# Optimization experiments

Measured on AMD Instinct MI355X. Metric: run time of the kernel, lower is better.

The kernel has to match this reference:

```python
import jax, jax.numpy as jnp
import numpy as np

NEG_SLOPE = 0.1
K = 3  # kernel_size

def lrelu(x):
    return jnp.where(x >= 0, x, NEG_SLOPE * x)

def setup_inputs() -> dict:
    key = jax.random.key(0)
    ks = jax.random.split(key, 10)
    B, C, H, W = 16, 64, 128, 128
    DEG, RED = 512, 8
    s = 0.02
    return {
        "feat": jax.random.normal(ks[0], (B, C, H, W), jnp.float32),
        "deg": jax.random.normal(ks[1], (B, DEG, 8, 8), jnp.float32),
        # adaptive_size: Linear(deg_fsize -> C), no bias; torch weight [out,in]
        "W_size": jax.random.normal(ks[2], (C, DEG), jnp.float32) * s,
        # kernel net: Linear(C -> C//red), Linear(C//red -> C*K*K)
        "W_k1": jax.random.normal(ks[3], (C // RED, C), jnp.float32) * s,
        "W_k2": jax.random.normal(ks[4], (C * K * K, C // RED), jnp.float32) * s,
        # 1x1 conv C_in -> C_out with bias (stored as [out,in])
        "W_conv": jax.random.normal(ks[5], (C, C), jnp.float32) * s,
        "b_conv": jax.random.normal(ks[6], (C,), jnp.float32) * s,
        # CA layer: 1x1 conv deg_fsize -> C, then C -> C//red -> C
        "W_ac": jax.random.normal(ks[7], (C, DEG), jnp.float32) * s,
        "W_du1": jax.random.normal(ks[8], (C // RED, C), jnp.float32) * s,
        "W_du2": jax.random.normal(ks[9], (C, C // RED), jnp.float32) * s,
    }

def reference(feat, deg, W_size, W_k1, W_k2, W_conv, b_conv, W_ac, W_du1, W_du2):
    b, c, h, w = feat.shape
    # degradation pooled to a vector: AdaptiveAvgPool2d((1,1)) == mean over HW
    dvec = deg.mean(axis=(2, 3))                      # [B, deg_fsize]
    f = dvec @ W_size.T                               # [B, C]
    # per-sample dynamic depthwise kernels
    kern = lrelu(f @ W_k1.T) @ W_k2.T                 # [B, C*K*K]
    kern = kern.reshape(b * c, 1, K, K)               # [B*C, 1, K, K]
    out = jax.lax.conv_general_dilated(
        feat.reshape(1, b * c, h, w), kern,
        window_strides=(1, 1), padding=[((K - 1) // 2,) * 2] * 2,
        feature_group_count=b * c,
        dimension_numbers=("NCHW", "OIHW", "NCHW"))
    out = lrelu(out).reshape(b, c, h, w)
    # trailing 1x1 conv with bias
    out = jnp.einsum("bchw,oc->bohw", out, W_conv) + b_conv[None, :, None, None]
    # CA branch
    fa = dvec @ W_ac.T                                # [B, C]
    att = jax.nn.sigmoid(lrelu(fa @ W_du1.T) @ W_du2.T)  # [B, C_out]
    return out + feat * att[:, :, None, None]
```

## Files before the change

### kernel.cpp

```cpp
#include <hip/hip_runtime.h>
#include <math.h>

#define NEG_SLOPE 0.1f

typedef __attribute__((ext_vector_type(8))) short short8;
typedef __attribute__((ext_vector_type(4))) float floatx4;

__device__ __forceinline__ float lrelu(float x) { return x >= 0.0f ? x : NEG_SLOPE * x; }

__device__ __forceinline__ unsigned short f2bf(float x) {
  unsigned u = __float_as_uint(x);
  return (unsigned short)((u + 0x7fffu + ((u >> 16) & 1u)) >> 16);
}

__device__ __forceinline__ float wave_sum64(float v) {
  #pragma unroll
  for (int s = 32; s > 0; s >>= 1) v += __shfl_xor(v, s, 64);
  return v;
}

__global__ __launch_bounds__(256) void prep_kernel(
    const float* __restrict__ deg, const float* __restrict__ W_size,
    const float* __restrict__ W_k1, const float* __restrict__ W_k2,
    const float* __restrict__ W_ac, const float* __restrict__ W_du1,
    const float* __restrict__ W_du2, float* __restrict__ kern_ws,
    float* __restrict__ att_ws) {
  const int b = blockIdx.x;
  const int t = threadIdx.x;
  __shared__ float dvec[512];
  __shared__ float fbuf[64], fabuf[64];
  __shared__ float t1s[8], t2s[8];

  const float* degb = deg + (size_t)b * 32768;
  const int q = t & 3, r0 = t >> 2;

  float rs[8];
  #pragma unroll
  for (int u = 0; u < 8; ++u) {
    const float* rp = degb + (size_t)(r0 + u * 64) * 64 + q * 16;
    float4 x0 = *(const float4*)(rp);
    float4 x1 = *(const float4*)(rp + 4);
    float4 x2 = *(const float4*)(rp + 8);
    float4 x3 = *(const float4*)(rp + 12);
    rs[u] = (x0.x + x0.y + x0.z + x0.w) + (x1.x + x1.y + x1.z + x1.w) +
            (x2.x + x2.y + x2.z + x2.w) + (x3.x + x3.y + x3.z + x3.w);
  }
  #pragma unroll
  for (int u = 0; u < 8; ++u) {
    float s = rs[u];
    s += __shfl_xor(s, 1, 64);
    s += __shfl_xor(s, 2, 64);
    if (q == 0) dvec[r0 + u * 64] = s * (1.0f / 64.0f);
  }
  __syncthreads();

  {
    const int c = t >> 2;
    const float* ws = W_size + (size_t)c * 512;
    const float* wa = W_ac + (size_t)c * 512;
    float p1 = 0.0f, p2 = 0.0f;
    #pragma unroll 4
    for (int k = 0; k < 32; ++k) {
      const int e = q * 4 + k * 16;
      float4 d  = *(const float4*)&dvec[e];
      float4 w1 = *(const float4*)(ws + e);
      float4 w2 = *(const float4*)(wa + e);
      p1 += d.x * w1.x + d.y * w1.y + d.z * w1.z + d.w * w1.w;
      p2 += d.x * w2.x + d.y * w2.y + d.z * w2.z + d.w * w2.w;
    }
    p1 += __shfl_xor(p1, 1, 64); p1 += __shfl_xor(p1, 2, 64);
    p2 += __shfl_xor(p2, 1, 64); p2 += __shfl_xor(p2, 2, 64);
    if (q == 0) { fbuf[c] = p1; fabuf[c] = p2; }
  }
  __syncthreads();

  const int wave = t >> 6, lane = t & 63;
  if (wave == 0) {
    float v = fbuf[lane];
    #pragma unroll
    for (int rr = 0; rr < 8; ++rr) {
      float p = wave_sum64(v * W_k1[rr * 64 + lane]);
      if (lane == 0) t1s[rr] = lrelu(p);
    }
  } else if (wave == 1) {
    float v = fabuf[lane];
    #pragma unroll
    for (int rr = 0; rr < 8; ++rr) {
      float p = wave_sum64(v * W_du1[rr * 64 + lane]);
      if (lane == 0) t2s[rr] = lrelu(p);
    }
  }
  __syncthreads();

  for (int i = t; i < 576; i += 256) {
    float4 wa0 = *(const float4*)&W_k2[i * 8];
    float4 wa1 = *(const float4*)&W_k2[i * 8 + 4];
    float s = t1s[0] * wa0.x + t1s[1] * wa0.y + t1s[2] * wa0.z + t1s[3] * wa0.w +
              t1s[4] * wa1.x + t1s[5] * wa1.y + t1s[6] * wa1.z + t1s[7] * wa1.w;
    kern_ws[b * 576 + i] = s;
  }
  if (t < 64) {
    float4 wa0 = *(const float4*)&W_du2[t * 8];
    float4 wa1 = *(const float4*)&W_du2[t * 8 + 4];
    float s = t2s[0] * wa0.x + t2s[1] * wa0.y + t2s[2] * wa0.z + t2s[3] * wa0.w +
              t2s[4] * wa1.x + t2s[5] * wa1.y + t2s[6] * wa1.z + t2s[7] * wa1.w;
    att_ws[b * 64 + t] = 1.0f / (1.0f + expf(-s));
  }
}

__global__ __launch_bounds__(256, 4) void fused_kernel(
    const float* __restrict__ feat, const float* __restrict__ W_conv,
    const float* __restrict__ b_conv, const float* __restrict__ kern_ws,
    const float* __restrict__ att_ws, float* __restrict__ out) {
  const int L = blockIdx.y * 128 + blockIdx.x;
  const int xcd = L & 7;
  const int rr_ = L >> 3;
  const int h = xcd * 16 + (rr_ & 15);
  const int b = rr_ >> 4;

  const int t = threadIdx.x;

  __shared__ __align__(16) unsigned short zT[128 * 72];
  __shared__ __align__(16) unsigned short wt[64 * 72];
  __shared__ float ks[576];
  __shared__ float atts[64];
  __shared__ float bcs[64];

  {
    const int o = t >> 2;
    const int c0 = (t & 3) * 16;
    const float* wp = W_conv + o * 64 + c0;
    float4 a0 = *(const float4*)(wp);
    float4 a1 = *(const float4*)(wp + 4);
    float4 a2 = *(const float4*)(wp + 8);
    float4 a3 = *(const float4*)(wp + 12);
    const int sw = (o >> 2) & 7;
    short8 p0, p1;
    p0[0] = f2bf(a0.x); p0[1] = f2bf(a0.y); p0[2] = f2bf(a0.z); p0[3] = f2bf(a0.w);
    p0[4] = f2bf(a1.x); p0[5] = f2bf(a1.y); p0[6] = f2bf(a1.z); p0[7] = f2bf(a1.w);
    p1[0] = f2bf(a2.x); p1[1] = f2bf(a2.y); p1[2] = f2bf(a2.z); p1[3] = f2bf(a2.w);
    p1[4] = f2bf(a3.x); p1[5] = f2bf(a3.y); p1[6] = f2bf(a3.z); p1[7] = f2bf(a3.w);
    const int kc0 = (c0 >> 3) ^ sw;
    const int kc1 = ((c0 >> 3) + 1) ^ sw;
    *(short8*)&wt[o * 72 + kc0 * 8] = p0;
    *(short8*)&wt[o * 72 + kc1 * 8] = p1;
  }
  for (int i = t; i < 576; i += 256) ks[i] = kern_ws[b * 576 + i];
  if (t < 64) { atts[t] = att_ws[b * 64 + t]; bcs[t] = b_conv[t]; }
  __syncthreads();

  const size_t base_b = (size_t)b * 64 * 128 * 128;

  {
    const int c8 = t & 7;
    const int gg = t >> 3;
    const int w0 = gg * 4;
    const int swz = gg & 7;

    #pragma unroll
    for (int it = 0; it < 8; ++it) {
      const int c = c8 + 8 * it;
      const float* kc = &ks[c * 9];
      const float k0 = kc[0], k1 = kc[1], k2 = kc[2];
      const float k3 = kc[3], k4 = kc[4], k5 = kc[5];
      const float k6 = kc[6], k7 = kc[7], k8 = kc[8];
      float a0 = 0.0f, a1 = 0.0f, a2 = 0.0f, a3 = 0.0f;
      const float* fc = feat + base_b + (size_t)c * 16384;

      auto row_acc = [&](const float* rowp, float ka, float kb, float kcv) {
        float4 m = *(const float4*)(rowp + w0);
        float left  = (w0 > 0)   ? rowp[w0 - 1] : 0.0f;
        float right = (w0 < 124) ? rowp[w0 + 4] : 0.0f;
        a0 += ka * left + kb * m.x + kcv * m.y;
        a1 += ka * m.x  + kb * m.y + kcv * m.z;
        a2 += ka * m.y  + kb * m.z + kcv * m.w;
        a3 += ka * m.z  + kb * m.w + kcv * right;
      };
      if (h > 0)   row_acc(fc + (size_t)(h - 1) * 128, k0, k1, k2);
                   row_acc(fc + (size_t)h * 128,       k3, k4, k5);
      if (h < 127) row_acc(fc + (size_t)(h + 1) * 128, k6, k7, k8);

      const int cbase = ((it ^ swz) * 8) + c8;
      zT[(w0 + 0) * 72 + cbase] = f2bf(lrelu(a0));
      zT[(w0 + 1) * 72 + cbase] = f2bf(lrelu(a1));
      zT[(w0 + 2) * 72 + cbase] = f2bf(lrelu(a2));
      zT[(w0 + 3) * 72 + cbase] = f2bf(lrelu(a3));
    }
  }
  __syncthreads();

  {
    const int lane = t & 63, wave = t >> 6;
    const int r = lane & 15, q = lane >> 4;
    const int m0 = wave * 16;

    short8 afrag[2];
    #pragma unroll
    for (int ksp = 0; ksp < 2; ++ksp) {
      const int o = m0 + r;
      const int kc = (ksp * 4 + q) ^ ((o >> 2) & 7);
      afrag[ksp] = *(const short8*)&wt[o * 72 + kc * 8];
    }

    floatx4 acc[8];
    #pragma unroll
    for (int nt = 0; nt < 8; ++nt) acc[nt] = (floatx4){0.f, 0.f, 0.f, 0.f};

    #pragma unroll
    for (int nt = 0; nt < 8; ++nt) {
      const int w = nt * 16 + r;
      const int sw = (w >> 2) & 7;
      #pragma unroll
      for (int ksp = 0; ksp < 2; ++ksp) {
        const int kc = (ksp * 4 + q) ^ sw;
        short8 bfrag = *(const short8*)&zT[w * 72 + kc * 8];
        acc[nt] = __builtin_amdgcn_mfma_f32_16x16x32_bf16(afrag[ksp], bfrag,
                                                          acc[nt], 0, 0, 0);
      }
    }

    #pragma unroll
    for (int nt = 0; nt < 8; ++nt) {
      const int w = nt * 16 + r;
      #pragma unroll
      for (int reg = 0; reg < 4; ++reg) {
        const int o = m0 + q * 4 + reg;
        const size_t idx = base_b + (size_t)o * 16384 + (size_t)h * 128 + w;
        out[idx] = acc[nt][reg] + bcs[o] + atts[o] * feat[idx];
      }
    }
  }
}

extern "C" void kernel_launch(void* const* d_in, const int* in_sizes, int n_in,
                              void* d_out, int out_size, void* d_ws, size_t ws_size,
                              hipStream_t stream) {
  const float* feat   = (const float*)d_in[0];
  const float* deg    = (const float*)d_in[1];
  const float* W_size = (const float*)d_in[2];
  const float* W_k1   = (const float*)d_in[3];
  const float* W_k2   = (const float*)d_in[4];
  const float* W_conv = (const float*)d_in[5];
  const float* b_conv = (const float*)d_in[6];
  const float* W_ac   = (const float*)d_in[7];
  const float* W_du1  = (const float*)d_in[8];
  const float* W_du2  = (const float*)d_in[9];
  float* out = (float*)d_out;

  float* kern_ws = (float*)d_ws;
  float* att_ws  = kern_ws + 16 * 576;

  prep_kernel<<<16, 256, 0, stream>>>(deg, W_size, W_k1, W_k2, W_ac, W_du1,
                                      W_du2, kern_ws, att_ws);
  fused_kernel<<<dim3(128, 16), 256, 0, stream>>>(feat, W_conv, b_conv,
                                                  kern_ws, att_ws, out);
}
```

Before: 183.6 us.

## Split prep into three parallel kernels and restructure fused conv with two rows per block

```diff
diff --git a/kernel.cpp b/kernel.cpp
--- a/kernel.cpp
+++ b/kernel.cpp
@@ -4,6 +4,7 @@
 #define NEG_SLOPE 0.1f
 
 typedef __attribute__((ext_vector_type(8))) short short8;
+typedef __attribute__((ext_vector_type(4))) short short4v;
 typedef __attribute__((ext_vector_type(4))) float floatx4;
 
 __device__ __forceinline__ float lrelu(float x) { return x >= 0.0f ? x : NEG_SLOPE * x; }
@@ -19,71 +20,78 @@
   return v;
 }
 
-__global__ __launch_bounds__(256) void prep_kernel(
-    const float* __restrict__ deg, const float* __restrict__ W_size,
+__global__ __launch_bounds__(256) void prep1_kernel(
+    const float* __restrict__ deg, float* __restrict__ dvec_ws) {
+  const int k = blockIdx.x;
+  const int b = k >> 2, quar = k & 3;
+  const int t = threadIdx.x;
+  const int rw = t >> 1, half = t & 1;
+  const int d = quar * 128 + rw;
+  const float* p = deg + (size_t)b * 32768 + (size_t)d * 64 + half * 32;
+  float4 x0 = *(const float4*)(p);
+  float4 x1 = *(const float4*)(p + 4);
+  float4 x2 = *(const float4*)(p + 8);
+  float4 x3 = *(const float4*)(p + 12);
+  float4 x4 = *(const float4*)(p + 16);
+  float4 x5 = *(const float4*)(p + 20);
+  float4 x6 = *(const float4*)(p + 24);
+  float4 x7 = *(const float4*)(p + 28);
+  float s = (x0.x + x0.y + x0.z + x0.w) + (x1.x + x1.y + x1.z + x1.w) +
+            (x2.x + x2.y + x2.z + x2.w) + (x3.x + x3.y + x3.z + x3.w) +
+            (x4.x + x4.y + x4.z + x4.w) + (x5.x + x5.y + x5.z + x5.w) +
+            (x6.x + x6.y + x6.z + x6.w) + (x7.x + x7.y + x7.z + x7.w);
+  s += __shfl_xor(s, 1, 64);
+  if (half == 0) dvec_ws[b * 512 + d] = s * (1.0f / 64.0f);
+}
+
+__global__ __launch_bounds__(256) void prep2_kernel(
+    const float* __restrict__ dvec_ws, const float* __restrict__ W_size,
+    const float* __restrict__ W_ac, float* __restrict__ f_ws,
+    float* __restrict__ fa_ws) {
+  const int k = blockIdx.x;
+  const int b = k >> 2, cq = k & 3;
+  const int t = threadIdx.x;
+  const int cl = t >> 4, sub = t & 15;
+  const int c = cq * 16 + cl;
+  const float* dv = dvec_ws + b * 512;
+  const float* w1 = W_size + (size_t)c * 512;
+  const float* w2 = W_ac + (size_t)c * 512;
+  float p1 = 0.0f, p2 = 0.0f;
+  #pragma unroll
+  for (int kk = 0; kk < 8; ++kk) {
+    const int e = sub * 4 + kk * 64;
+    float4 d  = *(const float4*)(dv + e);
+    float4 a  = *(const float4*)(w1 + e);
+    float4 bq = *(const float4*)(w2 + e);
+    p1 += d.x * a.x + d.y * a.y + d.z * a.z + d.w * a.w;
+    p2 += d.x * bq.x + d.y * bq.y + d.z * bq.z + d.w * bq.w;
+  }
+  #pragma unroll
+  for (int s = 1; s < 16; s <<= 1) {
+    p1 += __shfl_xor(p1, s, 64);
+    p2 += __shfl_xor(p2, s, 64);
+  }
+  if (sub == 0) { f_ws[b * 64 + c] = p1; fa_ws[b * 64 + c] = p2; }
+}
+
+__global__ __launch_bounds__(256) void prep3_kernel(
+    const float* __restrict__ f_ws, const float* __restrict__ fa_ws,
     const float* __restrict__ W_k1, const float* __restrict__ W_k2,
-    const float* __restrict__ W_ac, const float* __restrict__ W_du1,
-    const float* __restrict__ W_du2, float* __restrict__ kern_ws,
-    float* __restrict__ att_ws) {
+    const float* __restrict__ W_du1, const float* __restrict__ W_du2,
+    float* __restrict__ kern_ws, float* __restrict__ att_ws) {
   const int b = blockIdx.x;
   const int t = threadIdx.x;
-  __shared__ float dvec[512];
-  __shared__ float fbuf[64], fabuf[64];
   __shared__ float t1s[8], t2s[8];
-
-  const float* degb = deg + (size_t)b * 32768;
-  const int q = t & 3, r0 = t >> 2;
-
-  float rs[8];
-  #pragma unroll
-  for (int u = 0; u < 8; ++u) {
-    const float* rp = degb + (size_t)(r0 + u * 64) * 64 + q * 16;
-    float4 x0 = *(const float4*)(rp);
-    float4 x1 = *(const float4*)(rp + 4);
-    float4 x2 = *(const float4*)(rp + 8);
-    float4 x3 = *(const float4*)(rp + 12);
-    rs[u] = (x0.x + x0.y + x0.z + x0.w) + (x1.x + x1.y + x1.z + x1.w) +
-            (x2.x + x2.y + x2.z + x2.w) + (x3.x + x3.y + x3.z + x3.w);
-  }
-  #pragma unroll
-  for (int u = 0; u < 8; ++u) {
-    float s = rs[u];
-    s += __shfl_xor(s, 1, 64);
-    s += __shfl_xor(s, 2, 64);
-    if (q == 0) dvec[r0 + u * 64] = s * (1.0f / 64.0f);
-  }
-  __syncthreads();
-
-  {
-    const int c = t >> 2;
-    const float* ws = W_size + (size_t)c * 512;
-    const float* wa = W_ac + (size_t)c * 512;
-    float p1 = 0.0f, p2 = 0.0f;
-    #pragma unroll 4
-    for (int k = 0; k < 32; ++k) {
-      const int e = q * 4 + k * 16;
-      float4 d  = *(const float4*)&dvec[e];
-      float4 w1 = *(const float4*)(ws + e);
-      float4 w2 = *(const float4*)(wa + e);
-      p1 += d.x * w1.x + d.y * w1.y + d.z * w1.z + d.w * w1.w;
-      p2 += d.x * w2.x + d.y * w2.y + d.z * w2.z + d.w * w2.w;
-    }
-    p1 += __shfl_xor(p1, 1, 64); p1 += __shfl_xor(p1, 2, 64);
-    p2 += __shfl_xor(p2, 1, 64); p2 += __shfl_xor(p2, 2, 64);
-    if (q == 0) { fbuf[c] = p1; fabuf[c] = p2; }
-  }
-  __syncthreads();
-
   const int wave = t >> 6, lane = t & 63;
   if (wave == 0) {
-    float v = fbuf[lane];
+    float v = f_ws[b * 64 + lane];
     #pragma unroll
     for (int rr = 0; rr < 8; ++rr) {
       float p = wave_sum64(v * W_k1[rr * 64 + lane]);
       if (lane == 0) t1s[rr] = lrelu(p);
     }
   } else if (wave == 1) {
-    float v = fabuf[lane];
+    float v = fa_ws[b * 64 + lane];
     #pragma unroll
     for (int rr = 0; rr < 8; ++rr) {
       float p = wave_sum64(v * W_du1[rr * 64 + lane]);
@@ -91,13 +99,12 @@
     }
   }
   __syncthreads();
-
   for (int i = t; i < 576; i += 256) {
     float4 wa0 = *(const float4*)&W_k2[i * 8];
     float4 wa1 = *(const float4*)&W_k2[i * 8 + 4];
-    float s = t1s[0] * wa0.x + t1s[1] * wa0.y + t1s[2] * wa0.z + t1s[3] * wa0.w +
-              t1s[4] * wa1.x + t1s[5] * wa1.y + t1s[6] * wa1.z + t1s[7] * wa1.w;
-    kern_ws[b * 576 + i] = s;
+    kern_ws[b * 576 + i] =
+        t1s[0] * wa0.x + t1s[1] * wa0.y + t1s[2] * wa0.z + t1s[3] * wa0.w +
+        t1s[4] * wa1.x + t1s[5] * wa1.y + t1s[6] * wa1.z + t1s[7] * wa1.w;
   }
   if (t < 64) {
     float4 wa0 = *(const float4*)&W_du2[t * 8];
@@ -112,11 +119,12 @@
     const float* __restrict__ feat, const float* __restrict__ W_conv,
     const float* __restrict__ b_conv, const float* __restrict__ kern_ws,
     const float* __restrict__ att_ws, float* __restrict__ out) {
-  const int L = blockIdx.y * 128 + blockIdx.x;
-  const int xcd = L & 7;
-  const int rr_ = L >> 3;
-  const int h = xcd * 16 + (rr_ & 15);
-  const int b = rr_ >> 4;
+  const int bid = blockIdx.x;
+  const int xcd = bid & 7;
+  const int idx = bid >> 3;
+  const int b = idx >> 3;
+  const int sub = idx & 7;
+  const int h_base = xcd * 16 + sub * 2;
 
   const int t = threadIdx.x;
 
@@ -134,13 +142,13 @@
     float4 a1 = *(const float4*)(wp + 4);
     float4 a2 = *(const float4*)(wp + 8);
     float4 a3 = *(const float4*)(wp + 12);
-    const int sw = (o >> 2) & 7;
+    const int sw = ((o >> 2) ^ (o >> 5)) & 7;
     short8 p0, p1;
     p0[0] = f2bf(a0.x); p0[1] = f2bf(a0.y); p0[2] = f2bf(a0.z); p0[3] = f2bf(a0.w);
     p0[4] = f2bf(a1.x); p0[5] = f2bf(a1.y); p0[6] = f2bf(a1.z); p0[7] = f2bf(a1.w);
     p1[0] = f2bf(a2.x); p1[1] = f2bf(a2.y); p1[2] = f2bf(a2.z); p1[3] = f2bf(a2.w);
     p1[4] = f2bf(a3.x); p1[5] = f2bf(a3.y); p1[6] = f2bf(a3.z); p1[7] = f2bf(a3.w);
-    const int kc0 = (c0 >> 3) ^ sw;
+    const int kc0 = ((c0 >> 3) + 0) ^ sw;
     const int kc1 = ((c0 >> 3) + 1) ^ sw;
     *(short8*)&wt[o * 72 + kc0 * 8] = p0;
     *(short8*)&wt[o * 72 + kc1 * 8] = p1;
@@ -150,85 +158,143 @@
   __syncthreads();
 
   const size_t base_b = (size_t)b * 64 * 128 * 128;
-
-  {
-    const int c8 = t & 7;
-    const int gg = t >> 3;
-    const int w0 = gg * 4;
-    const int swz = gg & 7;
+  const int lane = t & 63, wave = t >> 6;
+  const int cq = t >> 5;
+  const int gg = t & 31;
+  const int w0 = gg * 4;
+  const int swz = (gg ^ (gg >> 3)) & 7;
+  const float4 zf4 = {0.f, 0.f, 0.f, 0.f};
+
+  #pragma unroll 1
+  for (int ti = 0; ti < 2; ++ti) {
+    const int h = h_base + ti;
+    const bool hgt0 = (h > 0), hlt = (h < 127);
+    const float* fbase = feat + base_b + (size_t)h * 128 + w0;
 
     #pragma unroll
-    for (int it = 0; it < 8; ++it) {
-      const int c = c8 + 8 * it;
-      const float* kc = &ks[c * 9];
-      const float k0 = kc[0], k1 = kc[1], k2 = kc[2];
-      const float k3 = kc[3], k4 = kc[4], k5 = kc[5];
-      const float k6 = kc[6], k7 = kc[7], k8 = kc[8];
-      float a0 = 0.0f, a1 = 0.0f, a2 = 0.0f, a3 = 0.0f;
-      const float* fc = feat + base_b + (size_t)c * 16384;
-
-      auto row_acc = [&](const float* rowp, float ka, float kb, float kcv) {
-        float4 m = *(const float4*)(rowp + w0);
-        float left  = (w0 > 0)   ? rowp[w0 - 1] : 0.0f;
-        float right = (w0 < 124) ? rowp[w0 + 4] : 0.0f;
-        a0 += ka * left + kb * m.x + kcv * m.y;
-        a1 += ka * m.x  + kb * m.y + kcv * m.z;
-        a2 += ka * m.y  + kb * m.z + kcv * m.w;
-        a3 += ka * m.z  + kb * m.w + kcv * right;
-      };
-      if (h > 0)   row_acc(fc + (size_t)(h - 1) * 128, k0, k1, k2);
-                   row_acc(fc + (size_t)h * 128,       k3, k4, k5);
-      if (h < 127) row_acc(fc + (size_t)(h + 1) * 128, k6, k7, k8);
-
-      const int cbase = ((it ^ swz) * 8) + c8;
-      zT[(w0 + 0) * 72 + cbase] = f2bf(lrelu(a0));
-      zT[(w0 + 1) * 72 + cbase] = f2bf(lrelu(a1));
-      zT[(w0 + 2) * 72 + cbase] = f2bf(lrelu(a2));
-      zT[(w0 + 3) * 72 + cbase] = f2bf(lrelu(a3));
+    for (int it = 0; it < 2; ++it) {
+      const int c0 = cq * 4 + it * 32;
+      float4 top[4], mid[4], bot[4];
+      #pragma unroll
+      for (int j = 0; j < 4; ++j) {
+        const float* p = fbase + (size_t)(c0 + j) * 16384;
+        mid[j] = *(const float4*)p;
+        top[j] = hgt0 ? *(const float4*)(p - 128) : zf4;
+        bot[j] = hlt  ? *(const float4*)(p + 128) : zf4;
+      }
+      unsigned short sres[4][4];
+      #pragma unroll
+      for (int j = 0; j < 4; ++j) {
+        const float* kv = &ks[(c0 + j) * 9];
+        const float k0 = kv[0], k1 = kv[1], k2 = kv[2];
+        const float k3 = kv[3], k4 = kv[4], k5 = kv[5];
+        const float k6 = kv[6], k7 = kv[7], k8 = kv[8];
+        float a0 = 0.f, a1 = 0.f, a2 = 0.f, a3 = 0.f;
+        {
+          float4 m = top[j];
+          float lf = __shfl(m.w, lane - 1, 64); if (gg == 0)  lf = 0.f;
+          float rt = __shfl(m.x, lane + 1, 64); if (gg == 31) rt = 0.f;
+          a0 += k0 * lf  + k1 * m.x + k2 * m.y;
+          a1 += k0 * m.x + k1 * m.y + k2 * m.z;
+          a2 += k0 * m.y + k1 * m.z + k2 * m.w;
+          a3 += k0 * m.z + k1 * m.w + k2 * rt;
+        }
+        {
+          float4 m = mid[j];
+          float lf = __shfl(m.w, lane - 1, 64); if (gg == 0)  lf = 0.f;
+          float rt = __shfl(m.x, lane + 1, 64); if (gg == 31) rt = 0.f;
+          a0 += k3 * lf  + k4 * m.x + k5 * m.y;
+          a1 += k3 * m.x + k4 * m.y + k5 * m.z;
+          a2 += k3 * m.y + k4 * m.z + k5 * m.w;
+          a3 += k3 * m.z + k4 * m.w + k5 * rt;
+        }
+        {
+          float4 m = bot[j];
+          float lf = __shfl(m.w, lane - 1, 64); if (gg == 0)  lf = 0.f;
+          float rt = __shfl(m.x, lane + 1, 64); if (gg == 31) rt = 0.f;
+          a0 += k6 * lf  + k7 * m.x + k8 * m.y;
+          a1 += k6 * m.x + k7 * m.y + k8 * m.z;
+          a2 += k6 * m.y + k7 * m.z + k8 * m.w;
+          a3 += k6 * m.z + k7 * m.w + k8 * rt;
+        }
+        sres[j][0] = f2bf(lrelu(a0));
+        sres[j][1] = f2bf(lrelu(a1));
+        sres[j][2] = f2bf(lrelu(a2));
+        sres[j][3] = f2bf(lrelu(a3));
+      }
+      const int chunk = (cq >> 1) + it * 4;
+      const int kcs = ((chunk ^ swz) * 8) + (cq & 1) * 4;
+      #pragma unroll
+      for (int i = 0; i < 4; ++i) {
+        short4v sv;
+        sv[0] = (short)sres[0][i]; sv[1] = (short)sres[1][i];
+        sv[2] = (short)sres[2][i]; sv[3] = (short)sres[3][i];
+        *(short4v*)&zT[(w0 + i) * 72 + kcs] = sv;
+      }
     }
-  }
-  __syncthreads();
-
-  {
-    const int lane = t & 63, wave = t >> 6;
-    const int r = lane & 15, q = lane >> 4;
-    const int m0 = wave * 16;
-
-    short8 afrag[2];
-    #pragma unroll
-    for (int ksp = 0; ksp < 2; ++ksp) {
-      const int o = m0 + r;
-      const int kc = (ksp * 4 + q) ^ ((o >> 2) & 7);
-      afrag[ksp] = *(const short8*)&wt[o * 72 + kc * 8];
+    __syncthreads();
+
+    {
+      const int r = lane & 15, q = lane >> 4;
+
+      short8 az[2][2];
+      #pragma unroll
+      for (int wm2 = 0; wm2 < 2; ++wm2) {
+        const int w = (wave * 2 + wm2) * 16 + r;
+        const int sz = ((w >> 2) ^ (w >> 5)) & 7;
+        #pragma unroll
+        for (int ksp = 0; ksp < 2; ++ksp) {
+          const int kc = (ksp * 4 + q) ^ sz;
+          az[wm2][ksp] = *(const short8*)&zT[w * 72 + kc * 8];
+        }
+      }
+      short8 bw[4][2];
+      #pragma unroll
+      for (int nt = 0; nt < 4; ++nt) {
+        const int o = nt * 16 + r;
+        const int so = ((o >> 2) ^ (o >> 5)) & 7;
+        #pragma unroll
+        for (int ksp = 0; ksp < 2; ++ksp) {
+          const int kc = (ksp * 4 + q) ^ so;
+          bw[nt][ksp] = *(const short8*)&wt[o * 72 + kc * 8];
+        }
+      }
+
+      floatx4 acc[2][4];
+      #pragma unroll
+      for (int wm2 = 0; wm2 < 2; ++wm2)
+        #pragma unroll
+        for (int nt = 0; nt < 4; ++nt) acc[wm2][nt] = (floatx4){0.f, 0.f, 0.f, 0.f};
+
+      #pragma unroll
+      for (int wm2 = 0; wm2 < 2; ++wm2)
+        #pragma unroll
+        for (int nt = 0; nt < 4; ++nt)
+          #pragma unroll
+          for (int ksp = 0; ksp < 2; ++ksp)
+            acc[wm2][nt] = __builtin_amdgcn_mfma_f32_16x16x32_bf16(
+                az[wm2][ksp], bw[nt][ksp], acc[wm2][nt], 0, 0, 0);
+
+      #pragma unroll
+      for (int wm2 = 0; wm2 < 2; ++wm2) {
+        const int wb = (wave * 2 + wm2) * 16 + q * 4;
+        #pragma unroll
+        for (int nt = 0; nt < 4; ++nt) {
+          const int o = nt * 16 + r;
+          const size_t off = base_b + (size_t)o * 16384 + (size_t)h * 128 + wb;
+          float4 fv = *(const float4*)(feat + off);
+          const float at = atts[o], bo = bcs[o];
+          floatx4 a = acc[wm2][nt];
+          float4 ov;
+          ov.x = a[0] + bo + at * fv.x;
+          ov.y = a[1] + bo + at * fv.y;
+          ov.z = a[2] + bo + at * fv.z;
+          ov.w = a[3] + bo + at * fv.w;
+          *(float4*)(out + off) = ov;
+        }
+      }
     }
-
-    floatx4 acc[8];
-    #pragma unroll
-    for (int nt = 0; nt < 8; ++nt) acc[nt] = (floatx4){0.f, 0.f, 0.f, 0.f};
-
-    #pragma unroll
-    for (int nt = 0; nt < 8; ++nt) {
-      const int w = nt * 16 + r;
-      const int sw = (w >> 2) & 7;
-      #pragma unroll
-      for (int ksp = 0; ksp < 2; ++ksp) {
-        const int kc = (ksp * 4 + q) ^ sw;
-        short8 bfrag = *(const short8*)&zT[w * 72 + kc * 8];
-        acc[nt] = __builtin_amdgcn_mfma_f32_16x16x32_bf16(afrag[ksp], bfrag,
-                                                          acc[nt], 0, 0, 0);
-      }
-    }
-
-    #pragma unroll
-    for (int nt = 0; nt < 8; ++nt) {
-      const int w = nt * 16 + r;
-      #pragma unroll
-      for (int reg = 0; reg < 4; ++reg) {
-        const int o = m0 + q * 4 + reg;
-        const size_t idx = base_b + (size_t)o * 16384 + (size_t)h * 128 + w;
-        out[idx] = acc[nt][reg] + bcs[o] + atts[o] * feat[idx];
-      }
-    }
+    if (ti == 0) __syncthreads();
   }
 }
 
@@ -247,11 +313,16 @@
   const float* W_du2  = (const float*)d_in[9];
   float* out = (float*)d_out;
 
-  float* kern_ws = (float*)d_ws;
+  float* dvec_ws = (float*)d_ws;
+  float* f_ws    = dvec_ws + 16 * 512;
+  float* fa_ws   = f_ws + 16 * 64;
+  float* kern_ws = fa_ws + 16 * 64;
   float* att_ws  = kern_ws + 16 * 576;
 
-  prep_kernel<<<16, 256, 0, stream>>>(deg, W_size, W_k1, W_k2, W_ac, W_du1,
-                                      W_du2, kern_ws, att_ws);
-  fused_kernel<<<dim3(128, 16), 256, 0, stream>>>(feat, W_conv, b_conv,
-                                                  kern_ws, att_ws, out);
-}
+  prep1_kernel<<<64, 256, 0, stream>>>(deg, dvec_ws);
+  prep2_kernel<<<64, 256, 0, stream>>>(dvec_ws, W_size, W_ac, f_ws, fa_ws);
+  prep3_kernel<<<16, 256, 0, stream>>>(f_ws, fa_ws, W_k1, W_k2, W_du1, W_du2,
+                                       kern_ws, att_ws);
+  fused_kernel<<<1024, 256, 0, stream>>>(feat, W_conv, b_conv, kern_ws, att_ws,
+                                         out);
+}
```

Measured after the change: 183.0 us. No clear change (-0.3%).
